# Kernel optimization log

Hardware: AMD Instinct MI355X
Metric: run time of the kernel (lower is better)

## Reference

```python
import jax, jax.numpy as jnp
import numpy as np


def setup_inputs() -> dict:
    key = jax.random.key(0)
    ks = jax.random.split(key, 8)
    B, Cin, H, W = 4, 256, 64, 64
    Ck = Cin // 2            # 128, KAN in/out dim
    NC = 21                  # num_classes
    return {
        "x": jax.random.normal(ks[0], (B, Cin, H, W), dtype=jnp.float32),
        "conv1_w": jax.random.normal(ks[1], (Ck, Cin, 3, 3), dtype=jnp.float32) * 0.02,
        "conv1_b": jnp.zeros((Ck,), dtype=jnp.float32),
        "kan_scale": jnp.ones((Ck, Ck), dtype=jnp.float32)
                     + 0.1 * jax.random.normal(ks[2], (Ck, Ck), dtype=jnp.float32),
        "kan_translation": 0.1 * jax.random.normal(ks[3], (Ck, Ck), dtype=jnp.float32),
        "kan_wavelet_weight": jax.random.normal(ks[4], (Ck, Ck), dtype=jnp.float32) * 0.1,
        "kan_base_weight": jax.random.normal(ks[5], (Ck, Ck), dtype=jnp.float32) * 0.05,
        "conv2_w": jax.random.normal(ks[6], (NC, Ck, 1, 1), dtype=jnp.float32) * 0.05,
        "conv2_b": jnp.zeros((NC,), dtype=jnp.float32),
    }


def _conv2d(x, w, b, pad):
    y = jax.lax.conv_general_dilated(
        x, w, window_strides=(1, 1), padding=pad,
        dimension_numbers=("NCHW", "OIHW", "NCHW"))
    return y + b[None, :, None, None]


def _wavelet_kan(x, scale, translation, wav_w, base_w):
    # x: (N, Cin). Wav-KAN (DoG) layer:
    #   u = (x - translation) / scale, per (out, in) pair -> (N, O, I)
    #   dog(u) = -u * exp(-u^2 / 2)
    #   wavelet_out[n, o] = sum_i dog(u)[n, o, i] * wav_w[o, i]
    #   base_out = silu(x) @ base_w.T
    u = (x[:, None, :] - translation[None]) / scale[None]          # (N, O, I)
    dog = -u * jnp.exp(-0.5 * u * u)                               # (N, O, I)
    wav_out = jnp.einsum("noi,oi->no", dog, wav_w)                 # (N, O)
    base_out = jnp.einsum("ni,oi->no", jax.nn.silu(x), base_w)     # (N, O)
    return wav_out + base_out


def reference(x, conv1_w, conv1_b, kan_scale, kan_translation,
              kan_wavelet_weight, kan_base_weight, conv2_w, conv2_b):
    h = jax.nn.relu(_conv2d(x, conv1_w, conv1_b, ((1, 1), (1, 1))))   # (B, Ck, H, W)
    B, C, H, W = h.shape
    flat = h.transpose(0, 2, 3, 1).reshape(B * H * W, C)              # (N, Ck)
    k = _wavelet_kan(flat, kan_scale, kan_translation,
                     kan_wavelet_weight, kan_base_weight)             # (N, Ck)
    k = k.reshape(B, H, W, -1).transpose(0, 3, 1, 2)                  # (B, Ck, H, W)
    return _conv2d(k, conv2_w, conv2_b, ((0, 0), (0, 0)))             # (B, NC, H, W)
```

## Files before the change

### kernel.cpp

```cpp
#include <hip/hip_runtime.h>
#include <math.h>

typedef __attribute__((ext_vector_type(8))) short s16x8;
typedef __attribute__((ext_vector_type(4))) float f32x4;
typedef __attribute__((ext_vector_type(2))) float f32x2;

#define LOG2E 1.4426950408889634f

#define OFF_XH   0
#define OFF_WB   2097152
#define OFF_PQT  2244608
#define OFF_W2   2310144
#define OFF_H    2315520

__global__ __launch_bounds__(256) void prep_all_k(
    const float* __restrict__ x, const float* __restrict__ w1,
    const float* __restrict__ ks, const float* __restrict__ kt,
    const float* __restrict__ kw, const float* __restrict__ kb,
    const float* __restrict__ w2, float* __restrict__ ws) {
  int blk = blockIdx.x;
  int t = threadIdx.x;
  if (blk < 1024) {
    __shared__ float lsm[64][65];
    unsigned short* xh = (unsigned short*)(ws + OFF_XH);
    int pr = blk & 63, cib = (blk >> 6) & 3, bb = blk >> 8;
    int sp0 = pr * 64;
    const float* src = x + (unsigned)(bb * 256 + cib * 64) * 4096 + sp0;
#pragma unroll
    for (int rr = 0; rr < 16; ++rr) {
      int idx = rr * 256 + t;
      int ci = idx >> 6, px = idx & 63;
      lsm[ci][px] = src[ci * 4096 + px];
    }
    __syncthreads();
#pragma unroll
    for (int rr = 0; rr < 16; ++rr) {
      int idx = rr * 256 + t;
      int px = idx >> 6, ci = idx & 63;
      unsigned u = __float_as_uint(lsm[ci][px]);
      xh[(unsigned)(bb * 4096 + sp0 + px) * 256 + cib * 64 + ci] =
          (unsigned short)((u + 0x7FFF + ((u >> 16) & 1)) >> 16);
    }
  } else if (blk < 2251) {
    int tid = (blk - 1024) * 256 + t;
    unsigned short* Wb = (unsigned short*)(ws + OFF_WB);
    if (tid < 294912) {
      int j = tid & 7, co = (tid >> 3) & 63, g = (tid >> 9) & 3, r = tid >> 11;
      int t9 = r % 9, q = r / 9, ck = q & 7, chh = q >> 3;
      int ci = ck * 32 + g * 8 + j, cog = chh * 64 + co;
      unsigned u = __float_as_uint(w1[(unsigned)(cog * 256 + ci) * 9 + t9]);
      Wb[tid] = (unsigned short)((u + 0x7FFF + ((u >> 16) & 1)) >> 16);
    } else if (tid < 294912 + 16384) {
      int i2 = tid - 294912;
      int i = i2 >> 7, o = i2 & 127;
      int ic = i >> 3, k = i & 7;
      float rs = 1.f / ks[o * 128 + i];
      float T  = kt[o * 128 + i];
      float A  = -0.7213475204444817f * rs * rs;
      float Bq = -2.f * A * T;
      float C  = A * T * T;
      float P0 = -rs * kw[o * 128 + i];
      float sc = exp2f(C);
      int khi = k >> 2, klo = k & 3;
      unsigned base = ((unsigned)ic * 8 * 128 + o) * 4 + klo;
      ws[OFF_PQT + base + (0 + khi) * 512] = A;
      ws[OFF_PQT + base + (2 + khi) * 512] = Bq;
      ws[OFF_PQT + base + (4 + khi) * 512] = P0 * sc;
      ws[OFF_PQT + base + (6 + khi) * 512] = -P0 * T * sc;
    } else if (tid < 294912 + 16384 + 2688) {
      int i3 = tid - 294912 - 16384;
      int nc = i3 >> 7, k = i3 & 127;
      ws[OFF_W2 + nc * 256 + k] = w2[nc * 128 + k];
    }
  } else {
    int nc = blk - 2251;
    if (t < 128) {
      float acc = 0.f;
      for (int o = 0; o < 128; ++o)
        acc = fmaf(w2[nc * 128 + o], kb[o * 128 + t], acc);
      ws[OFF_W2 + nc * 256 + 128 + t] = acc;
    }
  }
}

__global__ __launch_bounds__(256, 2) void conv1_mfma_k(
    const unsigned short* __restrict__ xh, const unsigned short* __restrict__ Wb,
    const float* __restrict__ b1, float* __restrict__ h) {
  __shared__ unsigned short Asm[3 * 66 * 40];
  __shared__ unsigned short Bsm[18432];
  int blk = blockIdx.x;
  int ch = blk & 1, y = (blk >> 1) & 63, bb = blk >> 7;
  int t = threadIdx.x;
  int wave = t >> 6, lane = t & 63;
  int wx = wave & 1, wn = wave >> 1;
  int l15 = lane & 15, lg = lane >> 4;

  if (t < 6) {
    int r = t >> 1, xl = (t & 1) * 65;
    float4 z = {0, 0, 0, 0};
    float4* p = (float4*)&Asm[(r * 66 + xl) * 40];
    p[0] = z; p[1] = z; p[2] = z; p[3] = z; p[4] = z;
  }

  f32x4 acc[2][2];
  f32x4 zz = {0.f, 0.f, 0.f, 0.f};
  acc[0][0] = zz; acc[0][1] = zz; acc[1][0] = zz; acc[1][1] = zz;

  int r_st = t >> 6, x_st = t & 63;
  int gy = y - 1 + r_st;
  bool arow = (r_st < 3);
  bool yok = arow & (gy >= 0) & (gy < 64);
  const unsigned short* asrc = xh + (unsigned)(bb * 4096 + gy * 64 + x_st) * 256;
  unsigned short* adst = &Asm[(r_st * 66 + x_st + 1) * 40];
  const unsigned short* bslab = Wb + ch * 8 * 18432;

  for (int ck = 0; ck < 8; ++ck) {
    float4 v0 = {0, 0, 0, 0}, v1 = v0, v2 = v0, v3 = v0;
    if (yok) {
      const float4* s = (const float4*)(asrc + ck * 32);
      v0 = s[0]; v1 = s[1]; v2 = s[2]; v3 = s[3];
    }
    if (arow) { float4* d = (float4*)adst; d[0] = v0; d[1] = v1; d[2] = v2; d[3] = v3; }
    {
      const float4* s = (const float4*)(bslab + ck * 18432);
      float4* d = (float4*)Bsm;
#pragma unroll
      for (int j = 0; j < 9; ++j) d[j * 256 + t] = s[j * 256 + t];
    }
    __syncthreads();
#pragma unroll
    for (int t9 = 0; t9 < 9; ++t9) {
      int ky = t9 / 3, kx = t9 % 3;
      s16x8 a[2], b[2];
      int abase = (ky * 66 + wx * 32 + l15 + kx) * 40 + lg * 8;
#pragma unroll
      for (int f = 0; f < 2; ++f)
        a[f] = *(const s16x8*)&Asm[abase + f * 640];
#pragma unroll
      for (int n = 0; n < 2; ++n)
        b[n] = *(const s16x8*)&Bsm[((t9 * 4 + lg) * 64 + wn * 32 + n * 16 + l15) * 8];
#pragma unroll
      for (int f = 0; f < 2; ++f)
#pragma unroll
        for (int n = 0; n < 2; ++n)
          acc[f][n] = __builtin_amdgcn_mfma_f32_16x16x32_bf16(a[f], b[n], acc[f][n], 0, 0, 0);
    }
    __syncthreads();
  }
#pragma unroll
  for (int n = 0; n < 2; ++n) {
    int co = ch * 64 + wn * 32 + n * 16 + l15;
    float bz = b1[co];
#pragma unroll
    for (int f = 0; f < 2; ++f) {
      int xbase = wx * 32 + f * 16 + lg * 4;
      float* dst = h + (unsigned)(bb * 4096 + y * 64 + xbase) * 128 + co;
#pragma unroll
      for (int r = 0; r < 4; ++r) {
        float v = acc[f][n][r] + bz;
        dst[r * 128] = v > 0.f ? v : 0.f;
      }
    }
  }
}

__global__ __launch_bounds__(128) void wavkan_k(
    const float* __restrict__ h, const float* __restrict__ PQT,
    float* __restrict__ kwout) {
  __shared__ float hsm[4][128];
  int n0 = blockIdx.x * 4;
  int t = threadIdx.x;
  {
    int row = t >> 5, c4 = (t & 31) * 4;
    *(float4*)&hsm[row][c4] = *(const float4*)&h[(unsigned)(n0 + row) * 128 + c4];
  }
  __syncthreads();

  int wave = t >> 6, lane = t & 63;
  int o = wave * 64 + lane;

  f32x2 accv[4];
#pragma unroll
  for (int n = 0; n < 4; ++n) accv[n] = (f32x2){0.f, 0.f};

  const float4* pq = (const float4*)PQT + o;

  for (int ic = 0; ic < 16; ++ic) {
    const float4* pp = pq + (unsigned)ic * 1024;
    float4 r0 = pp[0],   r1 = pp[128], r2 = pp[256], r3 = pp[384],
           r4 = pp[512], r5 = pp[640], r6 = pp[768], r7 = pp[896];
    f32x2 A2[4] = {{r0.x, r0.y}, {r0.z, r0.w}, {r1.x, r1.y}, {r1.z, r1.w}};
    f32x2 B2[4] = {{r2.x, r2.y}, {r2.z, r2.w}, {r3.x, r3.y}, {r3.z, r3.w}};
    f32x2 P2[4] = {{r4.x, r4.y}, {r4.z, r4.w}, {r5.x, r5.y}, {r5.z, r5.w}};
    f32x2 D2[4] = {{r6.x, r6.y}, {r6.z, r6.w}, {r7.x, r7.y}, {r7.z, r7.w}};
    int i0 = ic * 8;
#pragma unroll
    for (int n = 0; n < 4; ++n) {
      float4 h0 = *(const float4*)&hsm[n][i0];
      float4 h1 = *(const float4*)&hsm[n][i0 + 4];
      f32x2 hh[4] = {{h0.x, h0.y}, {h0.z, h0.w}, {h1.x, h1.y}, {h1.z, h1.w}};
      f32x2 a2 = accv[n];
#pragma unroll
      for (int q = 0; q < 4; ++q) {
        f32x2 h2 = hh[q];
        f32x2 t2 = A2[q] * h2 + B2[q];
        f32x2 u2 = t2 * h2;
        f32x2 e2;
        e2.x = __builtin_amdgcn_exp2f(u2.x);
        e2.y = __builtin_amdgcn_exp2f(u2.y);
        f32x2 v2 = P2[q] * h2 + D2[q];
        a2 = v2 * e2 + a2;
      }
      accv[n] = a2;
    }
  }
#pragma unroll
  for (int n = 0; n < 4; ++n)
    kwout[(unsigned)(n0 + n) * 128 + o] = accv[n].x + accv[n].y;
}

__global__ __launch_bounds__(256) void conv2_k(
    const float* __restrict__ kwv, const float* __restrict__ h,
    const float* __restrict__ w2c, const float* __restrict__ b2,
    float* __restrict__ out) {
  __shared__ float ksm[32][260];
  __shared__ float wsm[21 * 256];
  int n0 = blockIdx.x * 32;
  int t = threadIdx.x;
#pragma unroll 2
  for (int rr = 0; rr < 4; ++rr) {
    int idx4 = rr * 256 + t;
    int row = idx4 >> 5, c4 = (idx4 & 31) * 4;
    *(float4*)&ksm[row][c4] = *(const float4*)&kwv[(unsigned)(n0 + row) * 128 + c4];
    float4 v = *(const float4*)&h[(unsigned)(n0 + row) * 128 + c4];
    float4 s;
    s.x = v.x * __builtin_amdgcn_rcpf(1.f + __builtin_amdgcn_exp2f(-LOG2E * v.x));
    s.y = v.y * __builtin_amdgcn_rcpf(1.f + __builtin_amdgcn_exp2f(-LOG2E * v.y));
    s.z = v.z * __builtin_amdgcn_rcpf(1.f + __builtin_amdgcn_exp2f(-LOG2E * v.z));
    s.w = v.w * __builtin_amdgcn_rcpf(1.f + __builtin_amdgcn_exp2f(-LOG2E * v.w));
    *(float4*)&ksm[row][128 + c4] = s;
  }
#pragma unroll 2
  for (int j = t; j < 1344; j += 256)
    *(float4*)&wsm[j * 4] = *(const float4*)&w2c[j * 4];
  __syncthreads();

  int n = t & 31, ncg = t >> 5;
  float a0 = 0.f, a1 = 0.f, a2 = 0.f;
  bool has2 = ncg < 5;
#pragma unroll 4
  for (int i4 = 0; i4 < 64; ++i4) {
    float4 k4 = *(const float4*)&ksm[n][i4 * 4];
    float4 wA = *(const float4*)&wsm[ncg * 256 + i4 * 4];
    float4 wB = *(const float4*)&wsm[(ncg + 8) * 256 + i4 * 4];
    a0 += k4.x * wA.x + k4.y * wA.y + k4.z * wA.z + k4.w * wA.w;
    a1 += k4.x * wB.x + k4.y * wB.y + k4.z * wB.z + k4.w * wB.w;
    if (has2) {
      float4 wC = *(const float4*)&wsm[(ncg + 16) * 256 + i4 * 4];
      a2 += k4.x * wC.x + k4.y * wC.y + k4.z * wC.z + k4.w * wC.w;
    }
  }
  int gn = n0 + n, bb = gn >> 12, sp = gn & 4095;
  out[(unsigned)(bb * 21 + ncg) * 4096 + sp] = a0 + b2[ncg];
  out[(unsigned)(bb * 21 + ncg + 8) * 4096 + sp] = a1 + b2[ncg + 8];
  if (has2) out[(unsigned)(bb * 21 + ncg + 16) * 4096 + sp] = a2 + b2[ncg + 16];
}

extern "C" void kernel_launch(void* const* d_in, const int* in_sizes, int n_in,
                              void* d_out, int out_size, void* d_ws, size_t ws_size,
                              hipStream_t stream) {
  const float* x  = (const float*)d_in[0];
  const float* w1 = (const float*)d_in[1];
  const float* b1 = (const float*)d_in[2];
  const float* ks = (const float*)d_in[3];
  const float* kt = (const float*)d_in[4];
  const float* kw = (const float*)d_in[5];
  const float* kb = (const float*)d_in[6];
  const float* w2 = (const float*)d_in[7];
  const float* b2 = (const float*)d_in[8];
  float* out = (float*)d_out;
  float* ws  = (float*)d_ws;

  prep_all_k<<<2272, 256, 0, stream>>>(x, w1, ks, kt, kw, kb, w2, ws);
  conv1_mfma_k<<<512, 256, 0, stream>>>((const unsigned short*)(ws + OFF_XH),
                                        (const unsigned short*)(ws + OFF_WB),
                                        b1, ws + OFF_H);
  wavkan_k<<<4096, 128, 0, stream>>>(ws + OFF_H, ws + OFF_PQT,
                                     ws + OFF_XH );
  conv2_k<<<512, 256, 0, stream>>>(ws + OFF_XH, ws + OFF_H, ws + OFF_W2, b2, out);
}
```

Baseline: 92.79 us.

## Keep wavelet coefficients register-resident and split input dim across waves in wavkan

Restructures the wavelet KAN kernel so each block handles 64 rows and half the outputs, with each wave owning a 16-wide slice of the input dimension. The per-(o,i) coefficients stay in registers for the whole block and are no longer reloaded from global memory for every 4 rows. Partial sums are reduced across waves through shared memory. This trades repeated coefficient loads for extra LDS traffic, two barriers per tile, more registers and far fewer blocks.

New measurement: 90.71 us. -2.2%, faster.

```diff
diff --git a/kernel.cpp b/kernel.cpp
--- a/kernel.cpp
+++ b/kernel.cpp
@@ -164,59 +164,95 @@
   }
 }
 
-__global__ __launch_bounds__(128) void wavkan_k(
+__global__ __launch_bounds__(512) void wavkan_k(
     const float* __restrict__ h, const float* __restrict__ PQT,
     float* __restrict__ kwout) {
-  __shared__ float hsm[4][128];
-  int n0 = blockIdx.x * 4;
+  __shared__ float hsm[64][128];
+  __shared__ float part[8][8][64];
+  int blk = blockIdx.x;
+  int oh = blk & 1;
+  int n0 = (blk >> 1) * 64;
   int t = threadIdx.x;
+#pragma unroll
+  for (int rr = 0; rr < 4; ++rr) {
+    int idx4 = rr * 512 + t;
+    int row = idx4 >> 5, c4 = (idx4 & 31) * 4;
+    *(float4*)&hsm[row][c4] = *(const float4*)&h[(unsigned)(n0 + row) * 128 + c4];
+  }
+  int wave = t >> 6, lane = t & 63;
+  int o = oh * 64 + lane;
+  int i0 = wave * 16;
+  const float4* pq = (const float4*)PQT + o;
+  float4 pa[8], pb[8];
   {
-    int row = t >> 5, c4 = (t & 31) * 4;
-    *(float4*)&hsm[row][c4] = *(const float4*)&h[(unsigned)(n0 + row) * 128 + c4];
+    const float4* ppA = pq + (unsigned)(2 * wave) * 1024;
+    const float4* ppB = pq + (unsigned)(2 * wave + 1) * 1024;
+#pragma unroll
+    for (int j = 0; j < 8; ++j) pa[j] = ppA[j * 128];
+#pragma unroll
+    for (int j = 0; j < 8; ++j) pb[j] = ppB[j * 128];
   }
   __syncthreads();
 
-  int wave = t >> 6, lane = t & 63;
-  int o = wave * 64 + lane;
-
-  f32x2 accv[4];
-#pragma unroll
-  for (int n = 0; n < 4; ++n) accv[n] = (f32x2){0.f, 0.f};
-
-  const float4* pq = (const float4*)PQT + o;
-
-  for (int ic = 0; ic < 16; ++ic) {
-    const float4* pp = pq + (unsigned)ic * 1024;
-    float4 r0 = pp[0],   r1 = pp[128], r2 = pp[256], r3 = pp[384],
-           r4 = pp[512], r5 = pp[640], r6 = pp[768], r7 = pp[896];
-    f32x2 A2[4] = {{r0.x, r0.y}, {r0.z, r0.w}, {r1.x, r1.y}, {r1.z, r1.w}};
-    f32x2 B2[4] = {{r2.x, r2.y}, {r2.z, r2.w}, {r3.x, r3.y}, {r3.z, r3.w}};
-    f32x2 P2[4] = {{r4.x, r4.y}, {r4.z, r4.w}, {r5.x, r5.y}, {r5.z, r5.w}};
-    f32x2 D2[4] = {{r6.x, r6.y}, {r6.z, r6.w}, {r7.x, r7.y}, {r7.z, r7.w}};
-    int i0 = ic * 8;
-#pragma unroll
-    for (int n = 0; n < 4; ++n) {
-      float4 h0 = *(const float4*)&hsm[n][i0];
-      float4 h1 = *(const float4*)&hsm[n][i0 + 4];
-      f32x2 hh[4] = {{h0.x, h0.y}, {h0.z, h0.w}, {h1.x, h1.y}, {h1.z, h1.w}};
-      f32x2 a2 = accv[n];
-#pragma unroll
-      for (int q = 0; q < 4; ++q) {
-        f32x2 h2 = hh[q];
-        f32x2 t2 = A2[q] * h2 + B2[q];
-        f32x2 u2 = t2 * h2;
-        f32x2 e2;
-        e2.x = __builtin_amdgcn_exp2f(u2.x);
-        e2.y = __builtin_amdgcn_exp2f(u2.y);
-        f32x2 v2 = P2[q] * h2 + D2[q];
-        a2 = v2 * e2 + a2;
+  int rn = t >> 6, rl = t & 63;
+
+  for (int tile = 0; tile < 8; ++tile) {
+    int nb = tile * 8;
+#pragma unroll
+    for (int n = 0; n < 8; ++n) {
+      const float* hr = &hsm[nb + n][i0];
+      float4 h0 = *(const float4*)&hr[0];
+      float4 h1 = *(const float4*)&hr[4];
+      float4 h2 = *(const float4*)&hr[8];
+      float4 h3 = *(const float4*)&hr[12];
+      f32x2 a2 = (f32x2){0.f, 0.f};
+      {
+        f32x2 A2[4] = {{pa[0].x, pa[0].y}, {pa[0].z, pa[0].w}, {pa[1].x, pa[1].y}, {pa[1].z, pa[1].w}};
+        f32x2 B2[4] = {{pa[2].x, pa[2].y}, {pa[2].z, pa[2].w}, {pa[3].x, pa[3].y}, {pa[3].z, pa[3].w}};
+        f32x2 P2[4] = {{pa[4].x, pa[4].y}, {pa[4].z, pa[4].w}, {pa[5].x, pa[5].y}, {pa[5].z, pa[5].w}};
+        f32x2 D2[4] = {{pa[6].x, pa[6].y}, {pa[6].z, pa[6].w}, {pa[7].x, pa[7].y}, {pa[7].z, pa[7].w}};
+        f32x2 hh[4] = {{h0.x, h0.y}, {h0.z, h0.w}, {h1.x, h1.y}, {h1.z, h1.w}};
+#pragma unroll
+        for (int q = 0; q < 4; ++q) {
+          f32x2 hq = hh[q];
+          f32x2 t2 = A2[q] * hq + B2[q];
+          f32x2 u2 = t2 * hq;
+          f32x2 e2;
+          e2.x = __builtin_amdgcn_exp2f(u2.x);
+          e2.y = __builtin_amdgcn_exp2f(u2.y);
+          f32x2 v2 = P2[q] * hq + D2[q];
+          a2 = v2 * e2 + a2;
+        }
       }
-      accv[n] = a2;
-    }
-  }
-#pragma unroll
-  for (int n = 0; n < 4; ++n)
-    kwout[(unsigned)(n0 + n) * 128 + o] = accv[n].x + accv[n].y;
+      {
+        f32x2 A2[4] = {{pb[0].x, pb[0].y}, {pb[0].z, pb[0].w}, {pb[1].x, pb[1].y}, {pb[1].z, pb[1].w}};
+        f32x2 B2[4] = {{pb[2].x, pb[2].y}, {pb[2].z, pb[2].w}, {pb[3].x, pb[3].y}, {pb[3].z, pb[3].w}};
+        f32x2 P2[4] = {{pb[4].x, pb[4].y}, {pb[4].z, pb[4].w}, {pb[5].x, pb[5].y}, {pb[5].z, pb[5].w}};
+        f32x2 D2[4] = {{pb[6].x, pb[6].y}, {pb[6].z, pb[6].w}, {pb[7].x, pb[7].y}, {pb[7].z, pb[7].w}};
+        f32x2 hh[4] = {{h2.x, h2.y}, {h2.z, h2.w}, {h3.x, h3.y}, {h3.z, h3.w}};
+#pragma unroll
+        for (int q = 0; q < 4; ++q) {
+          f32x2 hq = hh[q];
+          f32x2 t2 = A2[q] * hq + B2[q];
+          f32x2 u2 = t2 * hq;
+          f32x2 e2;
+          e2.x = __builtin_amdgcn_exp2f(u2.x);
+          e2.y = __builtin_amdgcn_exp2f(u2.y);
+          f32x2 v2 = P2[q] * hq + D2[q];
+          a2 = v2 * e2 + a2;
+        }
+      }
+      part[wave][n][lane] = a2.x + a2.y;
+    }
+    __syncthreads();
+    {
+      float s = part[0][rn][rl];
+#pragma unroll
+      for (int j = 1; j < 8; ++j) s += part[j][rn][rl];
+      kwout[(unsigned)(n0 + nb + rn) * 128 + oh * 64 + rl] = s;
+    }
+    __syncthreads();
+  }
 }
 
 __global__ __launch_bounds__(256) void conv2_k(
@@ -285,7 +321,7 @@
   conv1_mfma_k<<<512, 256, 0, stream>>>((const unsigned short*)(ws + OFF_XH),
                                         (const unsigned short*)(ws + OFF_WB),
                                         b1, ws + OFF_H);
-  wavkan_k<<<4096, 128, 0, stream>>>(ws + OFF_H, ws + OFF_PQT,
-                                     ws + OFF_XH );
+  wavkan_k<<<512, 512, 0, stream>>>(ws + OFF_H, ws + OFF_PQT,
+                                    ws + OFF_XH );
   conv2_k<<<512, 256, 0, stream>>>(ws + OFF_XH, ws + OFF_H, ws + OFF_W2, b2, out);
 }
```

## Fuse conv1, wavelet-KAN and conv2 into a single per-row-tile kernel

Applied to the files above, without the earlier changes.

Merges the three post-prep kernels into one kernel in which each block computes a 32-pixel tile of conv1 over all 128 channels with MFMA, keeps the ReLU output in shared memory, evaluates the wavelet-KAN on it, and applies the 1x1 conv2 directly. This removes the global round trips of the intermediate h and KAN outputs and two kernel launches. In exchange, each block reloads every weight slab (both channel halves) with no cross-block sharing, the grid is only 512 blocks of 512 threads, and the wavelet stage now reads its parameter table from global memory for only 32 pixels per block.

Measured after the change: 97.77 us. 1.05x slower.

```diff
diff --git a/kernel.cpp b/kernel.cpp
--- a/kernel.cpp
+++ b/kernel.cpp
@@ -11,7 +11,6 @@
 #define OFF_WB   2097152
 #define OFF_PQT  2244608
 #define OFF_W2   2310144
-#define OFF_H    2315520
 
 __global__ __launch_bounds__(256) void prep_all_k(
     const float* __restrict__ x, const float* __restrict__ w1,
@@ -83,187 +82,179 @@
   }
 }
 
-__global__ __launch_bounds__(256, 2) void conv1_mfma_k(
+__global__ __launch_bounds__(512) void fused_k(
     const unsigned short* __restrict__ xh, const unsigned short* __restrict__ Wb,
-    const float* __restrict__ b1, float* __restrict__ h) {
-  __shared__ unsigned short Asm[3 * 66 * 40];
-  __shared__ unsigned short Bsm[18432];
+    const float* __restrict__ b1, const float* __restrict__ PQT,
+    const float* __restrict__ w2c, const float* __restrict__ b2,
+    float* __restrict__ out) {
+  __shared__ __align__(16) char smem[46080];
+  unsigned short* Asm = (unsigned short*)smem;
+  unsigned short* Bsm = (unsigned short*)(smem + 8160);
+  float* hsm = (float*)smem;
+  float* ksm = (float*)(smem + 16896);
+
   int blk = blockIdx.x;
-  int ch = blk & 1, y = (blk >> 1) & 63, bb = blk >> 7;
+  int xh2 = blk & 1, y = (blk >> 1) & 63, bb = blk >> 7;
+  int x0 = xh2 * 32;
   int t = threadIdx.x;
   int wave = t >> 6, lane = t & 63;
-  int wx = wave & 1, wn = wave >> 1;
+  int pxh = wave & 1, wc = wave >> 1;
   int l15 = lane & 15, lg = lane >> 4;
 
-  if (t < 6) {
-    int r = t >> 1, xl = (t & 1) * 65;
-    float4 z = {0, 0, 0, 0};
-    float4* p = (float4*)&Asm[(r * 66 + xl) * 40];
-    p[0] = z; p[1] = z; p[2] = z; p[3] = z; p[4] = z;
-  }
-
-  f32x4 acc[2][2];
-  f32x4 zz = {0.f, 0.f, 0.f, 0.f};
-  acc[0][0] = zz; acc[0][1] = zz; acc[1][0] = zz; acc[1][1] = zz;
-
-  int r_st = t >> 6, x_st = t & 63;
-  int gy = y - 1 + r_st;
-  bool arow = (r_st < 3);
-  bool yok = arow & (gy >= 0) & (gy < 64);
-  const unsigned short* asrc = xh + (unsigned)(bb * 4096 + gy * 64 + x_st) * 256;
-  unsigned short* adst = &Asm[(r_st * 66 + x_st + 1) * 40];
-  const unsigned short* bslab = Wb + ch * 8 * 18432;
+  f32x4 acc[2];
+  acc[0] = (f32x4){0.f, 0.f, 0.f, 0.f};
+  acc[1] = acc[0];
+
+  int arr = t / 136, arem = t % 136;
+  int acx = arem >> 2, aq = arem & 3;
+  int agy = y - 1 + arr, agx = x0 - 1 + acx;
+  bool aok = (t < 408) & (agy >= 0) & (agy < 64) & (agx >= 0) & (agx < 64);
+  const unsigned short* asrc =
+      xh + (unsigned)((bb * 4096 + agy * 64 + agx)) * 256 + aq * 8;
+  unsigned short* adst = Asm + ((arr * 34 + acx) * 40 + aq * 8);
 
   for (int ck = 0; ck < 8; ++ck) {
-    float4 v0 = {0, 0, 0, 0}, v1 = v0, v2 = v0, v3 = v0;
-    if (yok) {
-      const float4* s = (const float4*)(asrc + ck * 32);
-      v0 = s[0]; v1 = s[1]; v2 = s[2]; v3 = s[3];
-    }
-    if (arow) { float4* d = (float4*)adst; d[0] = v0; d[1] = v1; d[2] = v2; d[3] = v3; }
+    if (t < 408) {
+      float4 v = {0.f, 0.f, 0.f, 0.f};
+      if (aok) v = *(const float4*)(asrc + ck * 32);
+      *(float4*)adst = v;
+    }
     {
-      const float4* s = (const float4*)(bslab + ck * 18432);
+      const float4* s = (const float4*)(Wb + (unsigned)ck * 18432);
       float4* d = (float4*)Bsm;
-#pragma unroll
-      for (int j = 0; j < 9; ++j) d[j * 256 + t] = s[j * 256 + t];
+      for (int j = t; j < 2304; j += 512) d[j] = s[j];
     }
     __syncthreads();
 #pragma unroll
     for (int t9 = 0; t9 < 9; ++t9) {
       int ky = t9 / 3, kx = t9 % 3;
-      s16x8 a[2], b[2];
-      int abase = (ky * 66 + wx * 32 + l15 + kx) * 40 + lg * 8;
-#pragma unroll
-      for (int f = 0; f < 2; ++f)
-        a[f] = *(const s16x8*)&Asm[abase + f * 640];
-#pragma unroll
-      for (int n = 0; n < 2; ++n)
-        b[n] = *(const s16x8*)&Bsm[((t9 * 4 + lg) * 64 + wn * 32 + n * 16 + l15) * 8];
-#pragma unroll
-      for (int f = 0; f < 2; ++f)
-#pragma unroll
-        for (int n = 0; n < 2; ++n)
-          acc[f][n] = __builtin_amdgcn_mfma_f32_16x16x32_bf16(a[f], b[n], acc[f][n], 0, 0, 0);
-    }
-    __syncthreads();
-  }
-#pragma unroll
-  for (int n = 0; n < 2; ++n) {
-    int co = ch * 64 + wn * 32 + n * 16 + l15;
+      s16x8 a = *(const s16x8*)&Asm[(ky * 34 + pxh * 16 + l15 + kx) * 40 + lg * 8];
+      s16x8 b = *(const s16x8*)&Bsm[((t9 * 4 + lg) * 64 + wc * 16 + l15) * 8];
+      acc[0] = __builtin_amdgcn_mfma_f32_16x16x32_bf16(a, b, acc[0], 0, 0, 0);
+    }
+    __syncthreads();
+    {
+      const float4* s = (const float4*)(Wb + (unsigned)(8 + ck) * 18432);
+      float4* d = (float4*)Bsm;
+      for (int j = t; j < 2304; j += 512) d[j] = s[j];
+    }
+    __syncthreads();
+#pragma unroll
+    for (int t9 = 0; t9 < 9; ++t9) {
+      int ky = t9 / 3, kx = t9 % 3;
+      s16x8 a = *(const s16x8*)&Asm[(ky * 34 + pxh * 16 + l15 + kx) * 40 + lg * 8];
+      s16x8 b = *(const s16x8*)&Bsm[((t9 * 4 + lg) * 64 + wc * 16 + l15) * 8];
+      acc[1] = __builtin_amdgcn_mfma_f32_16x16x32_bf16(a, b, acc[1], 0, 0, 0);
+    }
+    __syncthreads();
+  }
+#pragma unroll
+  for (int pass = 0; pass < 2; ++pass) {
+    int co = pass * 64 + wc * 16 + l15;
     float bz = b1[co];
 #pragma unroll
-    for (int f = 0; f < 2; ++f) {
-      int xbase = wx * 32 + f * 16 + lg * 4;
-      float* dst = h + (unsigned)(bb * 4096 + y * 64 + xbase) * 128 + co;
-#pragma unroll
-      for (int r = 0; r < 4; ++r) {
-        float v = acc[f][n][r] + bz;
-        dst[r * 128] = v > 0.f ? v : 0.f;
+    for (int r = 0; r < 4; ++r) {
+      int px = pxh * 16 + lg * 4 + r;
+      float v = acc[pass][r] + bz;
+      hsm[px * 132 + co] = v > 0.f ? v : 0.f;
+    }
+  }
+  __syncthreads();
+
+  {
+    int oh = wave & 1, pg = wave >> 1;
+    int nb = pg * 8;
+    int o = oh * 64 + lane;
+    f32x2 accv[8];
+#pragma unroll
+    for (int n = 0; n < 8; ++n) accv[n] = (f32x2){0.f, 0.f};
+    const float4* pq = (const float4*)PQT + o;
+    for (int ic = 0; ic < 16; ++ic) {
+      const float4* pp = pq + (unsigned)ic * 1024;
+      float4 r0 = pp[0],   r1 = pp[128], r2 = pp[256], r3 = pp[384],
+             r4 = pp[512], r5 = pp[640], r6 = pp[768], r7 = pp[896];
+      f32x2 A2[4] = {{r0.x, r0.y}, {r0.z, r0.w}, {r1.x, r1.y}, {r1.z, r1.w}};
+      f32x2 B2[4] = {{r2.x, r2.y}, {r2.z, r2.w}, {r3.x, r3.y}, {r3.z, r3.w}};
+      f32x2 P2[4] = {{r4.x, r4.y}, {r4.z, r4.w}, {r5.x, r5.y}, {r5.z, r5.w}};
+      f32x2 D2[4] = {{r6.x, r6.y}, {r6.z, r6.w}, {r7.x, r7.y}, {r7.z, r7.w}};
+      int i0 = ic * 8;
+#pragma unroll
+      for (int n = 0; n < 8; ++n) {
+        const float* hr = &hsm[(nb + n) * 132 + i0];
+        float4 h0 = *(const float4*)&hr[0];
+        float4 h1 = *(const float4*)&hr[4];
+        f32x2 hh[4] = {{h0.x, h0.y}, {h0.z, h0.w}, {h1.x, h1.y}, {h1.z, h1.w}};
+        f32x2 a2 = accv[n];
+#pragma unroll
+        for (int q = 0; q < 4; ++q) {
+          f32x2 h2 = hh[q];
+          f32x2 t2 = A2[q] * h2 + B2[q];
+          f32x2 u2 = t2 * h2;
+          f32x2 e2;
+          e2.x = __builtin_amdgcn_exp2f(u2.x);
+          e2.y = __builtin_amdgcn_exp2f(u2.y);
+          f32x2 v2 = P2[q] * h2 + D2[q];
+          a2 = v2 * e2 + a2;
+        }
+        accv[n] = a2;
       }
     }
-  }
-}
-
-__global__ __launch_bounds__(128) void wavkan_k(
-    const float* __restrict__ h, const float* __restrict__ PQT,
-    float* __restrict__ kwout) {
-  __shared__ float hsm[4][128];
-  int n0 = blockIdx.x * 4;
-  int t = threadIdx.x;
+#pragma unroll
+    for (int n = 0; n < 8; ++n)
+      ksm[(nb + n) * 132 + o] = accv[n].x + accv[n].y;
+  }
+  __syncthreads();
+
   {
-    int row = t >> 5, c4 = (t & 31) * 4;
-    *(float4*)&hsm[row][c4] = *(const float4*)&h[(unsigned)(n0 + row) * 128 + c4];
+    int n = t >> 4, c8 = (t & 15) * 8;
+    float* hp = &hsm[n * 132 + c8];
+    float4 v0 = *(float4*)&hp[0], v1 = *(float4*)&hp[4];
+    float4 s0, s1;
+    s0.x = v0.x * __builtin_amdgcn_rcpf(1.f + __builtin_amdgcn_exp2f(-LOG2E * v0.x));
+    s0.y = v0.y * __builtin_amdgcn_rcpf(1.f + __builtin_amdgcn_exp2f(-LOG2E * v0.y));
+    s0.z = v0.z * __builtin_amdgcn_rcpf(1.f + __builtin_amdgcn_exp2f(-LOG2E * v0.z));
+    s0.w = v0.w * __builtin_amdgcn_rcpf(1.f + __builtin_amdgcn_exp2f(-LOG2E * v0.w));
+    s1.x = v1.x * __builtin_amdgcn_rcpf(1.f + __builtin_amdgcn_exp2f(-LOG2E * v1.x));
+    s1.y = v1.y * __builtin_amdgcn_rcpf(1.f + __builtin_amdgcn_exp2f(-LOG2E * v1.y));
+    s1.z = v1.z * __builtin_amdgcn_rcpf(1.f + __builtin_amdgcn_exp2f(-LOG2E * v1.z));
+    s1.w = v1.w * __builtin_amdgcn_rcpf(1.f + __builtin_amdgcn_exp2f(-LOG2E * v1.w));
+    *(float4*)&hp[0] = s0;
+    *(float4*)&hp[4] = s1;
   }
   __syncthreads();
 
-  int wave = t >> 6, lane = t & 63;
-  int o = wave * 64 + lane;
-
-  f32x2 accv[4];
-#pragma unroll
-  for (int n = 0; n < 4; ++n) accv[n] = (f32x2){0.f, 0.f};
-
-  const float4* pq = (const float4*)PQT + o;
-
-  for (int ic = 0; ic < 16; ++ic) {
-    const float4* pp = pq + (unsigned)ic * 1024;
-    float4 r0 = pp[0],   r1 = pp[128], r2 = pp[256], r3 = pp[384],
-           r4 = pp[512], r5 = pp[640], r6 = pp[768], r7 = pp[896];
-    f32x2 A2[4] = {{r0.x, r0.y}, {r0.z, r0.w}, {r1.x, r1.y}, {r1.z, r1.w}};
-    f32x2 B2[4] = {{r2.x, r2.y}, {r2.z, r2.w}, {r3.x, r3.y}, {r3.z, r3.w}};
-    f32x2 P2[4] = {{r4.x, r4.y}, {r4.z, r4.w}, {r5.x, r5.y}, {r5.z, r5.w}};
-    f32x2 D2[4] = {{r6.x, r6.y}, {r6.z, r6.w}, {r7.x, r7.y}, {r7.z, r7.w}};
-    int i0 = ic * 8;
-#pragma unroll
-    for (int n = 0; n < 4; ++n) {
-      float4 h0 = *(const float4*)&hsm[n][i0];
-      float4 h1 = *(const float4*)&hsm[n][i0 + 4];
-      f32x2 hh[4] = {{h0.x, h0.y}, {h0.z, h0.w}, {h1.x, h1.y}, {h1.z, h1.w}};
-      f32x2 a2 = accv[n];
-#pragma unroll
-      for (int q = 0; q < 4; ++q) {
-        f32x2 h2 = hh[q];
-        f32x2 t2 = A2[q] * h2 + B2[q];
-        f32x2 u2 = t2 * h2;
-        f32x2 e2;
-        e2.x = __builtin_amdgcn_exp2f(u2.x);
-        e2.y = __builtin_amdgcn_exp2f(u2.y);
-        f32x2 v2 = P2[q] * h2 + D2[q];
-        a2 = v2 * e2 + a2;
+  {
+    int n = t & 31, g = t >> 5;
+    bool has1 = g < 5;
+    const float* w0 = w2c + g * 256;
+    const float* w1p = w2c + (g + 16) * 256;
+    const float* kr = &ksm[n * 132];
+    const float* hr = &hsm[n * 132];
+    float a0 = 0.f, a1 = 0.f;
+#pragma unroll 4
+    for (int k4 = 0; k4 < 32; ++k4) {
+      float4 kv = *(const float4*)&kr[k4 * 4];
+      float4 w = *(const float4*)&w0[k4 * 4];
+      a0 += kv.x * w.x + kv.y * w.y + kv.z * w.z + kv.w * w.w;
+      if (has1) {
+        float4 wB = *(const float4*)&w1p[k4 * 4];
+        a1 += kv.x * wB.x + kv.y * wB.y + kv.z * wB.z + kv.w * wB.w;
       }
-      accv[n] = a2;
-    }
-  }
-#pragma unroll
-  for (int n = 0; n < 4; ++n)
-    kwout[(unsigned)(n0 + n) * 128 + o] = accv[n].x + accv[n].y;
-}
-
-__global__ __launch_bounds__(256) void conv2_k(
-    const float* __restrict__ kwv, const float* __restrict__ h,
-    const float* __restrict__ w2c, const float* __restrict__ b2,
-    float* __restrict__ out) {
-  __shared__ float ksm[32][260];
-  __shared__ float wsm[21 * 256];
-  int n0 = blockIdx.x * 32;
-  int t = threadIdx.x;
-#pragma unroll 2
-  for (int rr = 0; rr < 4; ++rr) {
-    int idx4 = rr * 256 + t;
-    int row = idx4 >> 5, c4 = (idx4 & 31) * 4;
-    *(float4*)&ksm[row][c4] = *(const float4*)&kwv[(unsigned)(n0 + row) * 128 + c4];
-    float4 v = *(const float4*)&h[(unsigned)(n0 + row) * 128 + c4];
-    float4 s;
-    s.x = v.x * __builtin_amdgcn_rcpf(1.f + __builtin_amdgcn_exp2f(-LOG2E * v.x));
-    s.y = v.y * __builtin_amdgcn_rcpf(1.f + __builtin_amdgcn_exp2f(-LOG2E * v.y));
-    s.z = v.z * __builtin_amdgcn_rcpf(1.f + __builtin_amdgcn_exp2f(-LOG2E * v.z));
-    s.w = v.w * __builtin_amdgcn_rcpf(1.f + __builtin_amdgcn_exp2f(-LOG2E * v.w));
-    *(float4*)&ksm[row][128 + c4] = s;
-  }
-#pragma unroll 2
-  for (int j = t; j < 1344; j += 256)
-    *(float4*)&wsm[j * 4] = *(const float4*)&w2c[j * 4];
-  __syncthreads();
-
-  int n = t & 31, ncg = t >> 5;
-  float a0 = 0.f, a1 = 0.f, a2 = 0.f;
-  bool has2 = ncg < 5;
+    }
 #pragma unroll 4
-  for (int i4 = 0; i4 < 64; ++i4) {
-    float4 k4 = *(const float4*)&ksm[n][i4 * 4];
-    float4 wA = *(const float4*)&wsm[ncg * 256 + i4 * 4];
-    float4 wB = *(const float4*)&wsm[(ncg + 8) * 256 + i4 * 4];
-    a0 += k4.x * wA.x + k4.y * wA.y + k4.z * wA.z + k4.w * wA.w;
-    a1 += k4.x * wB.x + k4.y * wB.y + k4.z * wB.z + k4.w * wB.w;
-    if (has2) {
-      float4 wC = *(const float4*)&wsm[(ncg + 16) * 256 + i4 * 4];
-      a2 += k4.x * wC.x + k4.y * wC.y + k4.z * wC.z + k4.w * wC.w;
-    }
-  }
-  int gn = n0 + n, bb = gn >> 12, sp = gn & 4095;
-  out[(unsigned)(bb * 21 + ncg) * 4096 + sp] = a0 + b2[ncg];
-  out[(unsigned)(bb * 21 + ncg + 8) * 4096 + sp] = a1 + b2[ncg + 8];
-  if (has2) out[(unsigned)(bb * 21 + ncg + 16) * 4096 + sp] = a2 + b2[ncg + 16];
+    for (int k4 = 0; k4 < 32; ++k4) {
+      float4 kv = *(const float4*)&hr[k4 * 4];
+      float4 w = *(const float4*)&w0[128 + k4 * 4];
+      a0 += kv.x * w.x + kv.y * w.y + kv.z * w.z + kv.w * w.w;
+      if (has1) {
+        float4 wB = *(const float4*)&w1p[128 + k4 * 4];
+        a1 += kv.x * wB.x + kv.y * wB.y + kv.z * wB.z + kv.w * wB.w;
+      }
+    }
+    int sp = y * 64 + x0 + n;
+    out[(unsigned)(bb * 21 + g) * 4096 + sp] = a0 + b2[g];
+    if (has1) out[(unsigned)(bb * 21 + g + 16) * 4096 + sp] = a1 + b2[g + 16];
+  }
 }
 
 extern "C" void kernel_launch(void* const* d_in, const int* in_sizes, int n_in,
@@ -282,10 +273,7 @@
   float* ws  = (float*)d_ws;
 
   prep_all_k<<<2272, 256, 0, stream>>>(x, w1, ks, kt, kw, kb, w2, ws);
-  conv1_mfma_k<<<512, 256, 0, stream>>>((const unsigned short*)(ws + OFF_XH),
-                                        (const unsigned short*)(ws + OFF_WB),
-                                        b1, ws + OFF_H);
-  wavkan_k<<<4096, 128, 0, stream>>>(ws + OFF_H, ws + OFF_PQT,
-                                     ws + OFF_XH );
-  conv2_k<<<512, 256, 0, stream>>>(ws + OFF_XH, ws + OFF_H, ws + OFF_W2, b2, out);
+  fused_k<<<512, 512, 0, stream>>>((const unsigned short*)(ws + OFF_XH),
+                                   (const unsigned short*)(ws + OFF_WB),
+                                   b1, ws + OFF_PQT, ws + OFF_W2, b2, out);
 }
```
